# Kernel tuning notes

Measured on AMD Instinct MI355X. Metric: run time of the kernel, lower is better.

The kernel has to match this reference:

```python
import jax, jax.numpy as jnp
import numpy as np

F_DIM = 64; HID = 256; P_ETA = 32; NBINS = 16; MULT = 3 * NBINS - 1
NLAYERS = 8; NBLOCKS = 2; TAIL = 10.0
MIN_BW = 1e-8; MIN_BH = 1e-8; MIN_D = 1e-8
THETA_DIM = F_DIM + 1
N_BATCH = 8192; M_DATA = 256


def _masks():
    in_deg = np.arange(1, F_DIM + 1)
    hid_deg = np.arange(HID) % (F_DIM - 1) + 1
    out_deg = np.repeat(in_deg, MULT)  # output index f*MULT+m has degree f+1
    m_in = (hid_deg[:, None] >= in_deg[None, :]).astype(np.float32)
    m_hh = (hid_deg[:, None] >= hid_deg[None, :]).astype(np.float32)
    m_out = (out_deg[:, None] > hid_deg[None, :]).astype(np.float32)
    return jnp.asarray(m_in), jnp.asarray(m_hh), jnp.asarray(m_out)


def _rqs_forward(x, uw, uh, ud):
    # unconstrained rational-quadratic spline with linear tails (nflows math)
    const = float(np.log(np.exp(1.0 - MIN_D) - 1.0))
    inside = (x >= -TAIL) & (x <= TAIL)
    ud = jnp.pad(ud, ((0, 0), (0, 0), (1, 1)), constant_values=const)  # [N,F,NBINS+1]
    w = jax.nn.softmax(uw, -1)
    w = MIN_BW + (1.0 - MIN_BW * NBINS) * w
    cw = jnp.concatenate([jnp.zeros_like(w[..., :1]), jnp.cumsum(w, -1)], -1)
    cw = 2.0 * TAIL * cw - TAIL
    cw = cw.at[..., 0].set(-TAIL).at[..., -1].set(TAIL)
    w = jnp.diff(cw, axis=-1)
    h = jax.nn.softmax(uh, -1)
    h = MIN_BH + (1.0 - MIN_BH * NBINS) * h
    ch = jnp.concatenate([jnp.zeros_like(h[..., :1]), jnp.cumsum(h, -1)], -1)
    ch = 2.0 * TAIL * ch - TAIL
    ch = ch.at[..., 0].set(-TAIL).at[..., -1].set(TAIL)
    h = jnp.diff(ch, axis=-1)
    d = MIN_D + jax.nn.softplus(ud)
    xs = jnp.clip(x, -TAIL, TAIL)
    idx = jnp.clip(jnp.sum((xs[..., None] >= cw).astype(jnp.int32), -1) - 1, 0, NBINS - 1)
    g = lambda a, i: jnp.take_along_axis(a, i[..., None], -1)[..., 0]
    icw, ich = g(cw, idx), g(ch, idx)
    iw, ih = g(w, idx), g(h, idx)
    delta = ih / iw
    d0, d1 = g(d, idx), g(d, idx + 1)
    t = (xs - icw) / iw
    tt = t * (1.0 - t)
    denom = delta + (d0 + d1 - 2.0 * delta) * tt
    y = ich + ih * (delta * t * t + d0 * tt) / denom
    dnum = delta * delta * (d1 * t * t + 2.0 * delta * tt + d0 * (1.0 - t) * (1.0 - t))
    ld = jnp.log(dnum) - 2.0 * jnp.log(denom)
    return jnp.where(inside, y, x), jnp.where(inside, ld, 0.0)


def _flow_transform(z, eta, W_in, b_in, W_ctx, b_ctx, W_blk, b_blk, W_out, b_out):
    m_in, m_hh, m_out = _masks()
    sqrt_h = jnp.sqrt(jnp.asarray(HID, z.dtype))

    def layer(carry, p):
        x, ld = carry
        Wi, bi, Wc, bc, Wb, bb, Wo, bo = p
        x = jnp.flip(x, axis=1)  # ReversePermutation (logdet 0)
        h = x @ (Wi * m_in).T + bi + eta @ Wc.T + bc  # MADE initial + context
        for k in range(NBLOCKS):  # masked pre-activation residual blocks
            t = jax.nn.relu(h)
            t = t @ (Wb[k, 0] * m_hh).T + bb[k, 0]
            t = jax.nn.relu(t)
            t = t @ (Wb[k, 1] * m_hh).T + bb[k, 1]
            h = h + t
        out = (h @ (Wo * m_out).T + bo).reshape(x.shape[0], F_DIM, MULT)
        uw = out[..., :NBINS] / sqrt_h
        uh = out[..., NBINS:2 * NBINS] / sqrt_h
        ud = out[..., 2 * NBINS:]
        x, l = _rqs_forward(x, uw, uh, ud)
        return (x, ld + l.sum(-1)), None

    init = (z, jnp.zeros(z.shape[0], z.dtype))
    (x, ld), _ = jax.lax.scan(layer, init, (W_in, b_in, W_ctx, b_ctx, W_blk, b_blk, W_out, b_out))
    return x, ld


def _stick_breaking(x):
    log_v = -jax.nn.softplus(-x)
    log_1v = -jax.nn.softplus(x)
    prefix = jnp.concatenate([jnp.zeros_like(x[:, :1]), jnp.cumsum(log_1v[:, :-1], 1)], 1)
    log_theta = jnp.concatenate([log_v + prefix, log_1v.sum(1, keepdims=True)], 1)
    wts = jnp.arange(F_DIM, 0, -1, dtype=x.dtype)
    log_det = log_v.sum(1) + (wts * log_1v).sum(1)
    return jnp.exp(log_theta), log_det


def setup_inputs() -> dict:
    key = jax.random.key(0)
    ks = jax.random.split(key, 8)
    s = 0.05
    return {
        'z': jax.random.normal(ks[0], (N_BATCH, F_DIM), jnp.float32),
        'eta_batch': jax.random.normal(ks[1], (N_BATCH, P_ETA), jnp.float32),
        'data_D2': jax.random.normal(ks[2], (M_DATA, THETA_DIM), jnp.float32),
        'W_in': s * jax.random.normal(ks[3], (NLAYERS, HID, F_DIM), jnp.float32),
        'b_in': jnp.zeros((NLAYERS, HID), jnp.float32),
        'W_ctx': s * jax.random.normal(ks[4], (NLAYERS, HID, P_ETA), jnp.float32),
        'b_ctx': jnp.zeros((NLAYERS, HID), jnp.float32),
        'W_blk': s * jax.random.normal(ks[5], (NLAYERS, NBLOCKS, 2, HID, HID), jnp.float32),
        'b_blk': jnp.zeros((NLAYERS, NBLOCKS, 2, HID), jnp.float32),
        'W_out': s * jax.random.normal(ks[6], (NLAYERS, F_DIM * MULT, HID), jnp.float32),
        'b_out': jnp.zeros((NLAYERS, F_DIM * MULT), jnp.float32),
    }


def reference(z, eta_batch, data_D2, W_in, b_in, W_ctx, b_ctx, W_blk, b_blk, W_out, b_out):
    x, flow_ld = _flow_transform(z, eta_batch, W_in, b_in, W_ctx, b_ctx, W_blk, b_blk, W_out, b_out)
    theta, sb_ld = _stick_breaking(x)
    total_ld = flow_ld + sb_ld
    log_qz = -0.5 * jnp.sum(z * z, -1) - 0.5 * F_DIM * jnp.log(2.0 * jnp.pi).astype(z.dtype)
    log_q = log_qz - total_ld
    # prior: Dirichlet(alpha=2) unnormalized: sum log(theta)
    log_p = jnp.sum(jnp.log(jnp.clip(theta, 1e-10, None)), -1)
    # likelihood: mean over data rows of isotropic Gaussian centered at theta
    d_sq = jnp.mean(jnp.sum(data_D2 * data_D2, -1))
    d_mean = jnp.mean(data_D2, 0)
    log_lik = -0.5 * (d_sq - 2.0 * theta @ d_mean + jnp.sum(theta * theta, -1))
    return jnp.mean(log_q - (log_p + log_lik))
```

## Files before the change

### kernel.cpp

```cpp
#include <hip/hip_runtime.h>
#include <math.h>

typedef float f32x4 __attribute__((ext_vector_type(4)));
typedef short bf16x8 __attribute__((ext_vector_type(8)));
typedef unsigned short u16;

typedef const __attribute__((address_space(1))) unsigned int ga_u32;
typedef __attribute__((address_space(3))) unsigned int ls_u32;

__device__ __forceinline__ void gl16(const void* g, void* l) {
    __builtin_amdgcn_global_load_lds((ga_u32*)g, (ls_u32*)l, 16, 0, 0);
}

__device__ __forceinline__ u16 f2bf(float f) {
    union { float f; unsigned u; } v; v.f = f;
    return (u16)((v.u + 0x7FFFu + ((v.u >> 16) & 1u)) >> 16);
}
__device__ __forceinline__ float bf2f(u16 h) {
    union { unsigned u; float f; } v; v.u = ((unsigned)h) << 16;
    return v.f;
}
__device__ __forceinline__ float splusf(float x) {
    return fmaxf(x, 0.f) + __logf(1.f + __expf(-fabsf(x)));
}
__device__ __forceinline__ int invperm(int k) {
    int m, q;
    if (k < 20) { m = k / 5; q = k - 5 * m; }
    else        { m = (k - 4) >> 2; q = (k - 4) & 3; }
    return m + 63 * q;
}

#define MID_ACT_P 264

__global__ __launch_bounds__(256) void setup_w(
    const float* __restrict__ Win, const float* __restrict__ bin,
    const float* __restrict__ Wctx, const float* __restrict__ bctx,
    const float* __restrict__ Wblk, const float* __restrict__ Wout,
    const float* __restrict__ bout, const float* __restrict__ eta,
    u16* __restrict__ W1, float* __restrict__ B1, u16* __restrict__ WB,
    float* __restrict__ BBp, u16* __restrict__ WO, float* __restrict__ BO,
    u16* __restrict__ AXE)
{
    const long N1 = 8L * 8 * 8 * 64 * 8;
    const long N2 = 8L * 256;
    const long N3 = 8L * 4 * 8 * 16 * 64 * 8;
    const long N3b = 8L * 4 * 256;
    const long N4 = 8L * 32 * 8 * 6 * 64 * 8;
    const long N5 = 8L * 3072;
    const long N6 = 8192L * 32;
    const long tot = N1 + N2 + N3 + N3b + N4 + N5 + N6;
    for (long i = (long)blockIdx.x * blockDim.x + threadIdx.x; i < tot;
         i += (long)gridDim.x * blockDim.x) {
        long t = i;
        if (t < N1) {
            int off = (int)(t & 7), lane = (int)((t >> 3) & 63);
            int frag = (int)((t >> 9) & 7), wv = (int)((t >> 12) & 7);
            long l = t >> 15;
            int ks = frag >> 1, f = frag & 1;
            int prow = wv * 32 + f * 16 + (lane & 15);
            int row = invperm(prow);
            int c = ks * 32 + ((lane >> 4) << 3) + off;
            float v = 0.f;
            if (c < 64)      v = Win[(l * 256 + row) * 64 + c] * (((row % 63) >= c) ? 1.f : 0.f);
            else if (c < 96) v = Wctx[(l * 256 + row) * 32 + (c - 64)];
            W1[t] = f2bf(v);
        } else if ((t -= N1) < N2) {
            long l = t >> 8; int k = (int)(t & 255);
            int c = invperm(k);
            B1[t] = bin[l * 256 + c] + bctx[l * 256 + c];
        } else if ((t -= N2) < N3) {
            int off = (int)(t & 7), lane = (int)((t >> 3) & 63);
            int frag = (int)((t >> 9) & 15), wv = (int)((t >> 13) & 7);
            int bi = (int)((t >> 16) & 3);
            long l = t >> 18;
            int prow = wv * 32 + (frag & 1) * 16 + (lane & 15);
            int pc   = ((frag >> 1) << 5) + ((lane >> 4) << 3) + off;
            int row = invperm(prow), c = invperm(pc);
            float v = Wblk[(((size_t)l * 4 + bi) * 256 + row) * 256 + c] *
                      (((row % 63) >= (c % 63)) ? 1.f : 0.f);
            WB[t] = f2bf(v);
        } else if ((t -= N3) < N3b) {
            long lb = t >> 8; int k = (int)(t & 255);
            (void)lb; (void)k;
        } else if ((t -= N3b) < N4) {
            long l = t / 786432; int rem = (int)(t % 786432);
            int y = rem / 24576, r2 = rem % 24576;
            int ks = r2 / 3072, r3 = r2 % 3072;
            int frag = r3 / 512, r4 = r3 % 512;
            int lane = r4 / 8, off = r4 % 8;
            int op = y * 96 + frag * 16 + (lane & 15);
            int pj = ks * 32 + ((lane >> 4) << 3) + off;
            int j = invperm(pj);
            int fd = op / 48, mm = op % 48;
            float v = 0.f;
            if (mm < 47 && fd > (j % 63))
                v = Wout[((size_t)l * 3008 + fd * 47 + mm) * 256 + j];
            WO[t] = f2bf(v);
        } else if ((t -= N4) < N5) {
            long l = t / 3072; int op = (int)(t % 3072);
            int fd = op / 48, mm = op % 48;
            BO[t] = (mm < 47) ? bout[l * 3008 + (long)fd * 47 + mm] : 0.f;
        } else {
            t -= N5;
            long b = t / 32; int p = (int)(t % 32);
            AXE[b * 96 + 64 + p] = f2bf(eta[t]);
        }
    }
}

__global__ __launch_bounds__(256) void perm_bias(
    const float* __restrict__ bblk, float* __restrict__ BBp)
{
    int t = blockIdx.x * 256 + threadIdx.x;
    int k = t & 255;
    BBp[t] = bblk[(t & ~255) | invperm(k)];
}

__global__ __launch_bounds__(128) void dstat(const float* __restrict__ D,
                                             float* __restrict__ DM)
{
    int j = threadIdx.x;
    float s = 0.f, q = 0.f;
    if (j < 65) {
        for (int m = 0; m < 256; ++m) {
            float v = D[m * 65 + j];
            s += v; q += v * v;
        }
        DM[j] = s * (1.f / 256.f);
    }
    __shared__ float red[128];
    red[j] = q; __syncthreads();
    for (int st = 64; st > 0; st >>= 1) {
        if (j < st) red[j] += red[j + st];
        __syncthreads();
    }
    if (j == 0) DM[65] = red[0] * (1.f / 256.f);
}

__global__ __launch_bounds__(256) void prep0(
    const float* __restrict__ z, float* __restrict__ XF, u16* __restrict__ AXE)
{
    size_t gt = (size_t)blockIdx.x * 256 + threadIdx.x;
    size_t b = gt >> 6; int f = (int)(gt & 63);
    float v = z[b * 64 + (63 - f)];
    XF[gt] = v;
    AXE[b * 96 + f] = f2bf(v);
}

template<int NF>
__device__ __forceinline__ void mid_stage_reg(
    const u16* __restrict__ gW, const u16* __restrict__ act,
    int lane, int fr, int kg, f32x4 (&T)[2])
{
    bf16x8 wf[NF];
#pragma unroll
    for (int j = 0; j < NF; ++j)
        wf[j] = *(const bf16x8*)(gW + (j * 64 + lane) * 8);
#pragma unroll
    for (int ks = 0; ks < NF / 2; ++ks) {
        bf16x8 af = *(const bf16x8*)&act[fr * MID_ACT_P + ks * 32 + kg * 8];
        T[0] = __builtin_amdgcn_mfma_f32_16x16x32_bf16(wf[ks * 2 + 0], af, T[0], 0, 0, 0);
        T[1] = __builtin_amdgcn_mfma_f32_16x16x32_bf16(wf[ks * 2 + 1], af, T[1], 0, 0, 0);
    }
}

__global__ __launch_bounds__(512) void fused_mid(
    const u16* __restrict__ AXE, const u16* __restrict__ W1l,
    const float* __restrict__ B1l, const u16* __restrict__ WBl,
    const float* __restrict__ bbl, u16* __restrict__ HB)
{
    __shared__ u16 act[16 * MID_ACT_P];
    const int tid = threadIdx.x;
    const int lane = tid & 63;
    const int wv = tid >> 6;
    const int fr = lane & 15, kg = lane >> 4;
    const int b0 = blockIdx.x * 16;
    const int ch0 = wv * 32;

    if (tid < 192) {
        int row = tid / 12, part = tid - row * 12;
        *(int4*)&act[row * MID_ACT_P + part * 8] =
            *(const int4*)&AXE[(size_t)(b0 + row) * 96 + part * 8];
    }

    f32x4 H[2], T[2];

    auto zeroT = [&]() {
        T[0] = (f32x4){0.f, 0.f, 0.f, 0.f};
        T[1] = (f32x4){0.f, 0.f, 0.f, 0.f};
    };
    auto epi = [&](const float* bias, int mode) {
#pragma unroll
        for (int m = 0; m < 2; ++m) {
            const int cb = ch0 + m * 16 + kg * 4;
            const float4 bs = *(const float4*)&bias[cb];
            f32x4 v = T[m];
            v[0] += bs.x; v[1] += bs.y; v[2] += bs.z; v[3] += bs.w;
            if (mode == 0) H[m] = v;
            if (mode == 2 || mode == 3) {
                H[m][0] += v[0]; H[m][1] += v[1];
                H[m][2] += v[2]; H[m][3] += v[3];
                v = H[m];
            }
            short4 q;
            if (mode != 3) {
                q.x = (short)f2bf(fmaxf(v[0], 0.f));
                q.y = (short)f2bf(fmaxf(v[1], 0.f));
                q.z = (short)f2bf(fmaxf(v[2], 0.f));
                q.w = (short)f2bf(fmaxf(v[3], 0.f));
                *(short4*)&act[fr * MID_ACT_P + cb] = q;
            } else {
                q.x = (short)f2bf(v[0]); q.y = (short)f2bf(v[1]);
                q.z = (short)f2bf(v[2]); q.w = (short)f2bf(v[3]);
                const int b = b0 + fr;
                const size_t idx =
                    (((((size_t)(b >> 7) * 8 + (cb >> 5)) * 8 + ((b >> 4) & 7)) * 64)
                     + (((cb >> 3) & 3) * 16 + (b & 15))) * 8 + (cb & 7);
                *(short4*)&HB[idx] = q;
            }
        }
    };

    zeroT();
    __syncthreads();
    mid_stage_reg<6>(W1l + wv * 4096, act, lane, fr, kg, T);
    __syncthreads();
    epi(B1l, 0);
    zeroT();
    __syncthreads();
    mid_stage_reg<16>(WBl + 0 * 65536 + wv * 8192, act, lane, fr, kg, T);
    __syncthreads();
    epi(bbl, 1);
    zeroT();
    __syncthreads();
    mid_stage_reg<16>(WBl + 1 * 65536 + wv * 8192, act, lane, fr, kg, T);
    __syncthreads();
    epi(bbl + 256, 2);
    zeroT();
    __syncthreads();
    mid_stage_reg<16>(WBl + 2 * 65536 + wv * 8192, act, lane, fr, kg, T);
    __syncthreads();
    epi(bbl + 2 * 256, 1);
    zeroT();
    __syncthreads();
    mid_stage_reg<16>(WBl + 3 * 65536 + wv * 8192, act, lane, fr, kg, T);
    __syncthreads();
    epi(bbl + 3 * 256, 3);
}

__global__ __launch_bounds__(256) void gemm_out_spline(
    const u16* __restrict__ A, const u16* __restrict__ Wo,
    const float* __restrict__ bo, const float* __restrict__ XF,
    float* __restrict__ Xn, float* __restrict__ XFnext, u16* __restrict__ AXE,
    float* __restrict__ LDP, int first)
{
    __shared__ u16 SM[14336];
    const int tid = threadIdx.x;
    const int lane = tid & 63, wv = tid >> 6;
    const int wm = wv >> 1, wn = wv & 1;
    const int fr = lane & 15, kg = lane >> 4;
    const int m0 = blockIdx.x * 128, n0 = blockIdx.y * 96;
    const int nk = ((int)blockIdx.y + 4) >> 2;

    u16* Ab = SM;
    u16* Bb = SM + 8192;

    const u16* gA = A  + (size_t)blockIdx.x * 32768;
    const u16* gB = Wo + (size_t)blockIdx.y * 24576;

    f32x4 acc[4][3];
#pragma unroll
    for (int m = 0; m < 4; ++m)
#pragma unroll
        for (int n = 0; n < 3; ++n) acc[m][n] = (f32x4){0.f, 0.f, 0.f, 0.f};

    gl16(gA + tid * 8,          Ab + tid * 8);
    gl16(gA + 2048 + tid * 8,   Ab + 2048 + tid * 8);
    gl16(gB + tid * 8,          Bb + tid * 8);
    if (tid < 128)
        gl16(gB + 2048 + tid * 8, Bb + 2048 + tid * 8);

    for (int ks = 0; ks < nk; ++ks) {
        __syncthreads();
        if (ks + 1 < nk) {
            const u16* sa = gA + (ks + 1) * 4096;
            const u16* sb = gB + (ks + 1) * 3072;
            u16* na = Ab + ((ks + 1) & 1) * 4096;
            u16* nb = Bb + ((ks + 1) & 1) * 3072;
            gl16(sa + tid * 8,          na + tid * 8);
            gl16(sa + 2048 + tid * 8,   na + 2048 + tid * 8);
            gl16(sb + tid * 8,          nb + tid * 8);
            if (tid < 128)
                gl16(sb + 2048 + tid * 8, nb + 2048 + tid * 8);
        }
        const u16* cA = Ab + (ks & 1) * 4096;
        const u16* cB = Bb + (ks & 1) * 3072;
        bf16x8 af[4], bf[3];
#pragma unroll
        for (int m = 0; m < 4; ++m)
            af[m] = *(const bf16x8*)&cA[(wm * 4 + m) * 512 + lane * 8];
#pragma unroll
        for (int n = 0; n < 3; ++n)
            bf[n] = *(const bf16x8*)&cB[(wn * 3 + n) * 512 + lane * 8];
#pragma unroll
        for (int m = 0; m < 4; ++m)
#pragma unroll
            for (int n = 0; n < 3; ++n)
                acc[m][n] = __builtin_amdgcn_mfma_f32_16x16x32_bf16(bf[n], af[m], acc[m][n], 0, 0, 0);
    }
    __syncthreads();

#pragma unroll
    for (int m = 0; m < 4; ++m) {
        const int row = wm * 64 + m * 16 + fr;
#pragma unroll
        for (int n = 0; n < 3; ++n) {
            const int c0 = wn * 48 + n * 16 + kg * 4;
            const float4 bs = *(const float4*)&bo[n0 + c0];
            short4 q;
            q.x = (short)f2bf(acc[m][n][0] + bs.x);
            q.y = (short)f2bf(acc[m][n][1] + bs.y);
            q.z = (short)f2bf(acc[m][n][2] + bs.z);
            q.w = (short)f2bf(acc[m][n][3] + bs.w);
            *(short4*)&SM[row * 104 + c0] = q;
        }
    }
    __syncthreads();

    const int r = tid >> 1, fi = tid & 1;
    const int b = m0 + r;
    const int fg = blockIdx.y * 2 + fi;
    const u16* o_ = &SM[r * 104 + fi * 48];
    bf16x8 v0 = *(const bf16x8*)(o_);
    bf16x8 v1 = *(const bf16x8*)(o_ + 8);
    bf16x8 v2 = *(const bf16x8*)(o_ + 16);
    bf16x8 v3 = *(const bf16x8*)(o_ + 24);
    bf16x8 v4 = *(const bf16x8*)(o_ + 32);
    bf16x8 v5 = *(const bf16x8*)(o_ + 40);

    float xin = XF[(size_t)b * 64 + fg];
    bool inside = (xin >= -10.f) && (xin <= 10.f);
    float xs = fminf(fmaxf(xin, -10.f), 10.f);

    float ew[16], eh[16], ud[15];
#pragma unroll
    for (int i = 0; i < 8; ++i) {
        ew[i]     = bf2f((u16)v0[i]) * 0.0625f;
        ew[8 + i] = bf2f((u16)v1[i]) * 0.0625f;
        eh[i]     = bf2f((u16)v2[i]) * 0.0625f;
        eh[8 + i] = bf2f((u16)v3[i]) * 0.0625f;
    }
#pragma unroll
    for (int i = 0; i < 8; ++i) ud[i] = bf2f((u16)v4[i]);
#pragma unroll
    for (int i = 0; i < 7; ++i) ud[8 + i] = bf2f((u16)v5[i]);

    float mw = ew[0], mh = eh[0];
#pragma unroll
    for (int i = 1; i < 16; ++i) { mw = fmaxf(mw, ew[i]); mh = fmaxf(mh, eh[i]); }
    float sw = 0.f, sh = 0.f;
#pragma unroll
    for (int i = 0; i < 16; ++i) {
        ew[i] = __expf(ew[i] - mw); sw += ew[i];
        eh[i] = __expf(eh[i] - mh); sh += eh[i];
    }
    const float kw = 20.f * (1.f - 1.6e-7f) / sw;
    const float kh = 20.f * (1.f - 1.6e-7f) / sh;

    float cwk = -10.f, chk = -10.f;
    float icw = -10.f, ich = -10.f, iw = 1.f, ih = 1.f, udl = 0.f, udr = 0.f;
    int selk = 0;
#pragma unroll
    for (int k = 0; k < 16; ++k) {
        const float cw1 = (k == 15) ? 10.f : cwk + (2e-7f + kw * ew[k]);
        const float ch1 = (k == 15) ? 10.f : chk + (2e-7f + kh * eh[k]);
        if (xs >= cwk) {
            selk = k;
            icw = cwk; iw = cw1 - cwk;
            ich = chk; ih = ch1 - chk;
            udl = (k >= 1)  ? ud[k - 1] : 0.f;
            udr = (k <= 14) ? ud[k]     : 0.f;
        }
        cwk = cw1; chk = ch1;
    }
    float d0 = (selk == 0)  ? 1.f : 1e-8f + splusf(udl);
    float d1 = (selk == 15) ? 1.f : 1e-8f + splusf(udr);
    float delta = ih / iw;
    float t = (xs - icw) / iw;
    float tt = t * (1.f - t);
    float denom = delta + (d0 + d1 - 2.f * delta) * tt;
    float y = ich + ih * (delta * t * t + d0 * tt) / denom;
    float omt = 1.f - t;
    float dnum = delta * delta * (d1 * t * t + 2.f * delta * tt + d0 * omt * omt);
    float ldv = __logf(dnum) - 2.f * __logf(denom);
    if (!inside) { y = xin; ldv = 0.f; }

    Xn[(size_t)b * 64 + fg] = y;
    XFnext[(size_t)b * 64 + (63 - fg)] = y;
    AXE[(size_t)b * 96 + (63 - fg)] = f2bf(y);

    float other = __shfl_xor(ldv, 1);
    if (fi == 0) {
        size_t o = (size_t)b * 32 + blockIdx.y;
        float v = ldv + other;
        LDP[o] = first ? v : (LDP[o] + v);
    }
}

__global__ __launch_bounds__(256) void final1(
    const float* __restrict__ X, const float* __restrict__ z,
    const float* __restrict__ LDP, const float* __restrict__ DM,
    float* __restrict__ PART)
{
    int tid = threadIdx.x;
    int b = blockIdx.x * 256 + tid;
    float ldt = 0.f;
    for (int g = 0; g < 32; ++g) ldt += LDP[(size_t)b * 32 + g];
    float pre = 0.f, lvs = 0.f, wls = 0.f, lp = 0.f, tdm = 0.f, tsq = 0.f;
    const float LCLIP = -23.02585093f;
    for (int i = 0; i < 64; ++i) {
        float xi = X[(size_t)b * 64 + i];
        float lv = -splusf(-xi), l1 = -splusf(xi);
        float lt = lv + pre;
        float th = __expf(lt);
        lp += fmaxf(lt, LCLIP);
        tdm += th * DM[i]; tsq += th * th;
        lvs += lv; wls += (float)(64 - i) * l1;
        pre += l1;
    }
    float th = __expf(pre);
    lp += fmaxf(pre, LCLIP); tdm += th * DM[64]; tsq += th * th;
    float zs = 0.f;
    for (int i = 0; i < 64; ++i) { float zz = z[(size_t)b * 64 + i]; zs += zz * zz; }
    float logqz = -0.5f * zs - 58.812066f;
    float log_q = logqz - (ldt + lvs + wls);
    float log_lik = -0.5f * (DM[65] - 2.f * tdm + tsq);
    float val = log_q - lp - log_lik;

    __shared__ float red[256];
    red[tid] = val; __syncthreads();
    for (int s = 128; s > 0; s >>= 1) {
        if (tid < s) red[tid] += red[tid + s];
        __syncthreads();
    }
    if (tid == 0) PART[blockIdx.x] = red[0];
}

__global__ __launch_bounds__(64) void final2(const float* __restrict__ PART,
                                             float* __restrict__ out)
{
    int tid = threadIdx.x;
    float s = (tid < 32) ? PART[tid] : 0.f;
    for (int o = 16; o > 0; o >>= 1) s += __shfl_down(s, o);
    if (tid == 0) out[0] = s * (1.f / 8192.f);
}

extern "C" void kernel_launch(void* const* d_in, const int* in_sizes, int n_in,
                              void* d_out, int out_size, void* d_ws, size_t ws_size,
                              hipStream_t stream)
{
    (void)in_sizes; (void)n_in; (void)out_size; (void)ws_size;
    const float* z    = (const float*)d_in[0];
    const float* eta  = (const float*)d_in[1];
    const float* dat  = (const float*)d_in[2];
    const float* Win  = (const float*)d_in[3];
    const float* bin  = (const float*)d_in[4];
    const float* Wctx = (const float*)d_in[5];
    const float* bctx = (const float*)d_in[6];
    const float* Wblk = (const float*)d_in[7];
    const float* bblk = (const float*)d_in[8];
    const float* Wout = (const float*)d_in[9];
    const float* bout = (const float*)d_in[10];
    float* out = (float*)d_out;

    char* w = (char*)d_ws;
    size_t off = 0;
    auto alloc = [&](size_t bytes) {
        void* p = w + off;
        off += (bytes + 255) & ~(size_t)255;
        return p;
    };
    u16*   W1  = (u16*)  alloc(8L * 32768 * 2);
    float* B1  = (float*)alloc(8L * 256 * 4);
    u16*   WB  = (u16*)  alloc(8L * 4 * 65536 * 2);
    float* BBp = (float*)alloc(8L * 4 * 256 * 4);
    u16*   WO  = (u16*)  alloc(8L * 786432 * 2);
    float* BO  = (float*)alloc(8L * 3072 * 4);
    u16*   AXE = (u16*)  alloc(8192L * 96 * 2);
    float* XFa = (float*)alloc(8192L * 64 * 4);
    float* XFb = (float*)alloc(8192L * 64 * 4);
    float* XC  = (float*)alloc(8192L * 64 * 4);
    u16*   HB  = (u16*)  alloc(8192L * 256 * 2);
    float* LDP = (float*)alloc(8192L * 32 * 4);
    float* DM  = (float*)alloc(66 * 4);
    float* PART= (float*)alloc(64 * 4);

    setup_w<<<dim3(2048), dim3(256), 0, stream>>>(
        Win, bin, Wctx, bctx, Wblk, Wout, bout, eta,
        W1, B1, WB, BBp, WO, BO, AXE);
    perm_bias<<<dim3(32), dim3(256), 0, stream>>>(bblk, BBp);
    dstat<<<dim3(1), dim3(128), 0, stream>>>(dat, DM);
    prep0<<<dim3(2048), dim3(256), 0, stream>>>(z, XFa, AXE);

    for (int l = 0; l < 8; ++l) {
        float* XFin  = (l & 1) ? XFb : XFa;
        float* XFout = (l & 1) ? XFa : XFb;
        fused_mid<<<dim3(512), dim3(512), 0, stream>>>(
            AXE, W1 + (size_t)l * 32768, B1 + l * 256,
            WB + (size_t)l * 262144, BBp + (size_t)l * 4 * 256, HB);
        gemm_out_spline<<<dim3(64, 32), dim3(256), 0, stream>>>(
            HB, WO + (size_t)l * 786432, BO + l * 3072, XFin,
            XC, XFout, AXE, LDP, (l == 0) ? 1 : 0);
    }
    final1<<<dim3(32), dim3(256), 0, stream>>>(XC, z, LDP, DM, PART);
    final2<<<dim3(1), dim3(64), 0, stream>>>(PART, out);
}
```

Measured before the change: 344.1 us.

## Switch all flow GEMMs from bf16 to fp8 e4m3 MFMA with scaled weights

```diff
diff --git a/kernel.cpp b/kernel.cpp
--- a/kernel.cpp
+++ b/kernel.cpp
@@ -1,9 +1,10 @@
 #include <hip/hip_runtime.h>
+#include <hip/hip_fp8.h>
 #include <math.h>
 
 typedef float f32x4 __attribute__((ext_vector_type(4)));
-typedef short bf16x8 __attribute__((ext_vector_type(8)));
 typedef unsigned short u16;
+typedef unsigned char u8;
 
 typedef const __attribute__((address_space(1))) unsigned int ga_u32;
 typedef __attribute__((address_space(3))) unsigned int ls_u32;
@@ -20,6 +21,12 @@
     union { unsigned u; float f; } v; v.u = ((unsigned)h) << 16;
     return v.f;
 }
+__device__ __forceinline__ u8 f2q(float f) {
+    __hip_fp8_e4m3 t(f);
+    return (u8)t.__x;
+}
+__device__ __forceinline__ long ld8(const u8* p) { return *(const long*)p; }
+
 __device__ __forceinline__ float splusf(float x) {
     return fmaxf(x, 0.f) + __logf(1.f + __expf(-fabsf(x)));
 }
@@ -30,25 +37,25 @@
     return m + 63 * q;
 }
 
-#define MID_ACT_P 264
+#define MID_ACT_P 272
+#define WSCALE 64.f
+#define WINV (1.f / 64.f)
 
 __global__ __launch_bounds__(256) void setup_w(
     const float* __restrict__ Win, const float* __restrict__ bin,
     const float* __restrict__ Wctx, const float* __restrict__ bctx,
     const float* __restrict__ Wblk, const float* __restrict__ Wout,
     const float* __restrict__ bout, const float* __restrict__ eta,
-    u16* __restrict__ W1, float* __restrict__ B1, u16* __restrict__ WB,
-    float* __restrict__ BBp, u16* __restrict__ WO, float* __restrict__ BO,
-    u16* __restrict__ AXE)
+    u8* __restrict__ W1, float* __restrict__ B1, u8* __restrict__ WB,
+    u8* __restrict__ WO, float* __restrict__ BO, u8* __restrict__ AXE)
 {
     const long N1 = 8L * 8 * 8 * 64 * 8;
     const long N2 = 8L * 256;
     const long N3 = 8L * 4 * 8 * 16 * 64 * 8;
-    const long N3b = 8L * 4 * 256;
     const long N4 = 8L * 32 * 8 * 6 * 64 * 8;
     const long N5 = 8L * 3072;
     const long N6 = 8192L * 32;
-    const long tot = N1 + N2 + N3 + N3b + N4 + N5 + N6;
+    const long tot = N1 + N2 + N3 + N4 + N5 + N6;
     for (long i = (long)blockIdx.x * blockDim.x + threadIdx.x; i < tot;
          i += (long)gridDim.x * blockDim.x) {
         long t = i;
@@ -63,7 +70,7 @@
             float v = 0.f;
             if (c < 64)      v = Win[(l * 256 + row) * 64 + c] * (((row % 63) >= c) ? 1.f : 0.f);
             else if (c < 96) v = Wctx[(l * 256 + row) * 32 + (c - 64)];
-            W1[t] = f2bf(v);
+            W1[t] = f2q(v * WSCALE);
         } else if ((t -= N1) < N2) {
             long l = t >> 8; int k = (int)(t & 255);
             int c = invperm(k);
@@ -78,11 +85,8 @@
             int row = invperm(prow), c = invperm(pc);
             float v = Wblk[(((size_t)l * 4 + bi) * 256 + row) * 256 + c] *
                       (((row % 63) >= (c % 63)) ? 1.f : 0.f);
-            WB[t] = f2bf(v);
-        } else if ((t -= N3) < N3b) {
-            long lb = t >> 8; int k = (int)(t & 255);
-            (void)lb; (void)k;
-        } else if ((t -= N3b) < N4) {
+            WB[t] = f2q(v * WSCALE);
+        } else if ((t -= N3) < N4) {
             long l = t / 786432; int rem = (int)(t % 786432);
             int y = rem / 24576, r2 = rem % 24576;
             int ks = r2 / 3072, r3 = r2 % 3072;
@@ -95,7 +99,7 @@
             float v = 0.f;
             if (mm < 47 && fd > (j % 63))
                 v = Wout[((size_t)l * 3008 + fd * 47 + mm) * 256 + j];
-            WO[t] = f2bf(v);
+            WO[t] = f2q(v * WSCALE);
         } else if ((t -= N4) < N5) {
             long l = t / 3072; int op = (int)(t % 3072);
             int fd = op / 48, mm = op % 48;
@@ -103,7 +107,7 @@
         } else {
             t -= N5;
             long b = t / 32; int p = (int)(t % 32);
-            AXE[b * 96 + 64 + p] = f2bf(eta[t]);
+            AXE[b * 96 + 64 + p] = f2q(eta[t]);
         }
     }
 }
@@ -138,38 +142,38 @@
 }
 
 __global__ __launch_bounds__(256) void prep0(
-    const float* __restrict__ z, float* __restrict__ XF, u16* __restrict__ AXE)
+    const float* __restrict__ z, float* __restrict__ XF, u8* __restrict__ AXE)
 {
     size_t gt = (size_t)blockIdx.x * 256 + threadIdx.x;
     size_t b = gt >> 6; int f = (int)(gt & 63);
     float v = z[b * 64 + (63 - f)];
     XF[gt] = v;
-    AXE[b * 96 + f] = f2bf(v);
+    AXE[b * 96 + f] = f2q(v);
 }
 
 template<int NF>
 __device__ __forceinline__ void mid_stage_reg(
-    const u16* __restrict__ gW, const u16* __restrict__ act,
+    const u8* __restrict__ gW, const u8* __restrict__ act,
     int lane, int fr, int kg, f32x4 (&T)[2])
 {
-    bf16x8 wf[NF];
+    long wf[NF];
 #pragma unroll
     for (int j = 0; j < NF; ++j)
-        wf[j] = *(const bf16x8*)(gW + (j * 64 + lane) * 8);
+        wf[j] = ld8(gW + (j * 64 + lane) * 8);
 #pragma unroll
     for (int ks = 0; ks < NF / 2; ++ks) {
-        bf16x8 af = *(const bf16x8*)&act[fr * MID_ACT_P + ks * 32 + kg * 8];
-        T[0] = __builtin_amdgcn_mfma_f32_16x16x32_bf16(wf[ks * 2 + 0], af, T[0], 0, 0, 0);
-        T[1] = __builtin_amdgcn_mfma_f32_16x16x32_bf16(wf[ks * 2 + 1], af, T[1], 0, 0, 0);
+        long af = ld8(&act[fr * MID_ACT_P + ks * 32 + kg * 8]);
+        T[0] = __builtin_amdgcn_mfma_f32_16x16x32_fp8_fp8(wf[ks * 2 + 0], af, T[0], 0, 0, 0);
+        T[1] = __builtin_amdgcn_mfma_f32_16x16x32_fp8_fp8(wf[ks * 2 + 1], af, T[1], 0, 0, 0);
     }
 }
 
 __global__ __launch_bounds__(512) void fused_mid(
-    const u16* __restrict__ AXE, const u16* __restrict__ W1l,
-    const float* __restrict__ B1l, const u16* __restrict__ WBl,
-    const float* __restrict__ bbl, u16* __restrict__ HB)
-{
-    __shared__ u16 act[16 * MID_ACT_P];
+    const u8* __restrict__ AXE, const u8* __restrict__ W1l,
+    const float* __restrict__ B1l, const u8* __restrict__ WBl,
+    const float* __restrict__ bbl, u8* __restrict__ HB)
+{
+    __shared__ u8 act[16 * MID_ACT_P];
     const int tid = threadIdx.x;
     const int lane = tid & 63;
     const int wv = tid >> 6;
@@ -177,10 +181,10 @@
     const int b0 = blockIdx.x * 16;
     const int ch0 = wv * 32;
 
-    if (tid < 192) {
-        int row = tid / 12, part = tid - row * 12;
-        *(int4*)&act[row * MID_ACT_P + part * 8] =
-            *(const int4*)&AXE[(size_t)(b0 + row) * 96 + part * 8];
+    if (tid < 96) {
+        int row = tid / 6, part = tid - row * 6;
+        *(int4*)&act[row * MID_ACT_P + part * 16] =
+            *(const int4*)&AXE[(size_t)(b0 + row) * 96 + part * 16];
     }
 
     f32x4 H[2], T[2];
@@ -195,28 +199,29 @@
             const int cb = ch0 + m * 16 + kg * 4;
             const float4 bs = *(const float4*)&bias[cb];
             f32x4 v = T[m];
-            v[0] += bs.x; v[1] += bs.y; v[2] += bs.z; v[3] += bs.w;
+            v[0] = v[0] * WINV + bs.x; v[1] = v[1] * WINV + bs.y;
+            v[2] = v[2] * WINV + bs.z; v[3] = v[3] * WINV + bs.w;
             if (mode == 0) H[m] = v;
             if (mode == 2 || mode == 3) {
                 H[m][0] += v[0]; H[m][1] += v[1];
                 H[m][2] += v[2]; H[m][3] += v[3];
                 v = H[m];
             }
-            short4 q;
+            unsigned pk;
             if (mode != 3) {
-                q.x = (short)f2bf(fmaxf(v[0], 0.f));
-                q.y = (short)f2bf(fmaxf(v[1], 0.f));
-                q.z = (short)f2bf(fmaxf(v[2], 0.f));
-                q.w = (short)f2bf(fmaxf(v[3], 0.f));
-                *(short4*)&act[fr * MID_ACT_P + cb] = q;
+                pk = (unsigned)f2q(fmaxf(v[0], 0.f))
+                   | ((unsigned)f2q(fmaxf(v[1], 0.f)) << 8)
+                   | ((unsigned)f2q(fmaxf(v[2], 0.f)) << 16)
+                   | ((unsigned)f2q(fmaxf(v[3], 0.f)) << 24);
+                *(unsigned*)&act[fr * MID_ACT_P + cb] = pk;
             } else {
-                q.x = (short)f2bf(v[0]); q.y = (short)f2bf(v[1]);
-                q.z = (short)f2bf(v[2]); q.w = (short)f2bf(v[3]);
+                pk = (unsigned)f2q(v[0]) | ((unsigned)f2q(v[1]) << 8)
+                   | ((unsigned)f2q(v[2]) << 16) | ((unsigned)f2q(v[3]) << 24);
                 const int b = b0 + fr;
                 const size_t idx =
                     (((((size_t)(b >> 7) * 8 + (cb >> 5)) * 8 + ((b >> 4) & 7)) * 64)
                      + (((cb >> 3) & 3) * 16 + (b & 15))) * 8 + (cb & 7);
-                *(short4*)&HB[idx] = q;
+                *(unsigned*)&HB[idx] = pk;
             }
         }
     };
@@ -249,24 +254,26 @@
 }
 
 __global__ __launch_bounds__(256) void gemm_out_spline(
-    const u16* __restrict__ A, const u16* __restrict__ Wo,
+    const u8* __restrict__ A, const u8* __restrict__ Wo,
     const float* __restrict__ bo, const float* __restrict__ XF,
-    float* __restrict__ Xn, float* __restrict__ XFnext, u16* __restrict__ AXE,
+    float* __restrict__ Xn, float* __restrict__ XFnext, u8* __restrict__ AXE,
     float* __restrict__ LDP, int first)
 {
-    __shared__ u16 SM[14336];
+    __shared__ u16 SM16[13312];
+    u8* SM8 = (u8*)SM16;
     const int tid = threadIdx.x;
     const int lane = tid & 63, wv = tid >> 6;
     const int wm = wv >> 1, wn = wv & 1;
     const int fr = lane & 15, kg = lane >> 4;
-    const int m0 = blockIdx.x * 128, n0 = blockIdx.y * 96;
-    const int nk = ((int)blockIdx.y + 4) >> 2;
-
-    u16* Ab = SM;
-    u16* Bb = SM + 8192;
-
-    const u16* gA = A  + (size_t)blockIdx.x * 32768;
-    const u16* gB = Wo + (size_t)blockIdx.y * 24576;
+    const int by = 31 - (int)blockIdx.y;
+    const int m0 = blockIdx.x * 128, n0 = by * 96;
+    const int nk = (by + 4) >> 2;
+
+    u8* Ab = SM8;
+    u8* Bb = SM8 + 8192;
+
+    const u8* gA = A  + (size_t)blockIdx.x * 16384;
+    const u8* gB = Wo + (size_t)by * 24576;
 
     f32x4 acc[4][3];
 #pragma unroll
@@ -274,39 +281,33 @@
 #pragma unroll
         for (int n = 0; n < 3; ++n) acc[m][n] = (f32x4){0.f, 0.f, 0.f, 0.f};
 
-    gl16(gA + tid * 8,          Ab + tid * 8);
-    gl16(gA + 2048 + tid * 8,   Ab + 2048 + tid * 8);
-    gl16(gB + tid * 8,          Bb + tid * 8);
-    if (tid < 128)
-        gl16(gB + 2048 + tid * 8, Bb + 2048 + tid * 8);
+    gl16(gA + tid * 16, Ab + tid * 16);
+    if (tid < 192) gl16(gB + tid * 16, Bb + tid * 16);
 
     for (int ks = 0; ks < nk; ++ks) {
         __syncthreads();
         if (ks + 1 < nk) {
-            const u16* sa = gA + (ks + 1) * 4096;
-            const u16* sb = gB + (ks + 1) * 3072;
-            u16* na = Ab + ((ks + 1) & 1) * 4096;
-            u16* nb = Bb + ((ks + 1) & 1) * 3072;
-            gl16(sa + tid * 8,          na + tid * 8);
-            gl16(sa + 2048 + tid * 8,   na + 2048 + tid * 8);
-            gl16(sb + tid * 8,          nb + tid * 8);
-            if (tid < 128)
-                gl16(sb + 2048 + tid * 8, nb + 2048 + tid * 8);
+            const u8* sa = gA + (ks + 1) * 4096;
+            const u8* sb = gB + (ks + 1) * 3072;
+            u8* na = Ab + ((ks + 1) & 1) * 4096;
+            u8* nb = Bb + ((ks + 1) & 1) * 3072;
+            gl16(sa + tid * 16, na + tid * 16);
+            if (tid < 192) gl16(sb + tid * 16, nb + tid * 16);
         }
-        const u16* cA = Ab + (ks & 1) * 4096;
-        const u16* cB = Bb + (ks & 1) * 3072;
-        bf16x8 af[4], bf[3];
+        const u8* cA = Ab + (ks & 1) * 4096;
+        const u8* cB = Bb + (ks & 1) * 3072;
+        long af[4], bf[3];
 #pragma unroll
         for (int m = 0; m < 4; ++m)
-            af[m] = *(const bf16x8*)&cA[(wm * 4 + m) * 512 + lane * 8];
+            af[m] = ld8(&cA[(wm * 4 + m) * 512 + lane * 8]);
 #pragma unroll
         for (int n = 0; n < 3; ++n)
-            bf[n] = *(const bf16x8*)&cB[(wn * 3 + n) * 512 + lane * 8];
+            bf[n] = ld8(&cB[(wn * 3 + n) * 512 + lane * 8]);
 #pragma unroll
         for (int m = 0; m < 4; ++m)
 #pragma unroll
             for (int n = 0; n < 3; ++n)
-                acc[m][n] = __builtin_amdgcn_mfma_f32_16x16x32_bf16(bf[n], af[m], acc[m][n], 0, 0, 0);
+                acc[m][n] = __builtin_amdgcn_mfma_f32_16x16x32_fp8_fp8(bf[n], af[m], acc[m][n], 0, 0, 0);
     }
     __syncthreads();
 
@@ -318,19 +319,20 @@
             const int c0 = wn * 48 + n * 16 + kg * 4;
             const float4 bs = *(const float4*)&bo[n0 + c0];
             short4 q;
-            q.x = (short)f2bf(acc[m][n][0] + bs.x);
-            q.y = (short)f2bf(acc[m][n][1] + bs.y);
-            q.z = (short)f2bf(acc[m][n][2] + bs.z);
-            q.w = (short)f2bf(acc[m][n][3] + bs.w);
-            *(short4*)&SM[row * 104 + c0] = q;
+            q.x = (short)f2bf(acc[m][n][0] * WINV + bs.x);
+            q.y = (short)f2bf(acc[m][n][1] * WINV + bs.y);
+            q.z = (short)f2bf(acc[m][n][2] * WINV + bs.z);
+            q.w = (short)f2bf(acc[m][n][3] * WINV + bs.w);
+            *(short4*)&SM16[row * 104 + c0] = q;
         }
     }
     __syncthreads();
 
+    typedef short bf16x8 __attribute__((ext_vector_type(8)));
     const int r = tid >> 1, fi = tid & 1;
     const int b = m0 + r;
-    const int fg = blockIdx.y * 2 + fi;
-    const u16* o_ = &SM[r * 104 + fi * 48];
+    const int fg = by * 2 + fi;
+    const u16* o_ = &SM16[r * 104 + fi * 48];
     bf16x8 v0 = *(const bf16x8*)(o_);
     bf16x8 v1 = *(const bf16x8*)(o_ + 8);
     bf16x8 v2 = *(const bf16x8*)(o_ + 16);
@@ -397,11 +399,11 @@
 
     Xn[(size_t)b * 64 + fg] = y;
     XFnext[(size_t)b * 64 + (63 - fg)] = y;
-    AXE[(size_t)b * 96 + (63 - fg)] = f2bf(y);
+    AXE[(size_t)b * 96 + (63 - fg)] = f2q(y);
 
     float other = __shfl_xor(ldv, 1);
     if (fi == 0) {
-        size_t o = (size_t)b * 32 + blockIdx.y;
+        size_t o = (size_t)b * 32 + by;
         float v = ldv + other;
         LDP[o] = first ? v : (LDP[o] + v);
     }
@@ -480,24 +482,24 @@
         off += (bytes + 255) & ~(size_t)255;
         return p;
     };
-    u16*   W1  = (u16*)  alloc(8L * 32768 * 2);
+    u8*    W1  = (u8*)   alloc(8L * 32768);
     float* B1  = (float*)alloc(8L * 256 * 4);
-    u16*   WB  = (u16*)  alloc(8L * 4 * 65536 * 2);
+    u8*    WB  = (u8*)   alloc(8L * 262144);
     float* BBp = (float*)alloc(8L * 4 * 256 * 4);
-    u16*   WO  = (u16*)  alloc(8L * 786432 * 2);
+    u8*    WO  = (u8*)   alloc(8L * 786432);
     float* BO  = (float*)alloc(8L * 3072 * 4);
-    u16*   AXE = (u16*)  alloc(8192L * 96 * 2);
+    u8*    AXE = (u8*)   alloc(8192L * 96);
     float* XFa = (float*)alloc(8192L * 64 * 4);
     float* XFb = (float*)alloc(8192L * 64 * 4);
     float* XC  = (float*)alloc(8192L * 64 * 4);
-    u16*   HB  = (u16*)  alloc(8192L * 256 * 2);
+    u8*    HB  = (u8*)   alloc(8192L * 256);
     float* LDP = (float*)alloc(8192L * 32 * 4);
     float* DM  = (float*)alloc(66 * 4);
     float* PART= (float*)alloc(64 * 4);
 
     setup_w<<<dim3(2048), dim3(256), 0, stream>>>(
         Win, bin, Wctx, bctx, Wblk, Wout, bout, eta,
-        W1, B1, WB, BBp, WO, BO, AXE);
+        W1, B1, WB, WO, BO, AXE);
     perm_bias<<<dim3(32), dim3(256), 0, stream>>>(bblk, BBp);
     dstat<<<dim3(1), dim3(128), 0, stream>>>(dat, DM);
     prep0<<<dim3(2048), dim3(256), 0, stream>>>(z, XFa, AXE);
```

Measured after the change: 314.6 us. 8.6% less time.
